# Kernel optimization log

Measured on AMD Instinct MI355X. Metric: run time of the kernel, lower is better.

Reference implementation:

```python
import math
import jax, jax.numpy as jnp
import numpy as np

N, E, EA = 25000, 400000, 400000
DN, DE, H = 256, 128, 8
DHN, DHE = DN // H, DE // H
EPS = 1e-5


def _ln(x, g, b):
    m = x.mean(-1, keepdims=True)
    v = ((x - m) ** 2).mean(-1, keepdims=True)
    return (x - m) * jax.lax.rsqrt(v + EPS) * g + b


def _scatter_softmax(scores, index, n):
    # per-segment stable softmax (matches torch scatter_reduce amax + scatter_add)
    m = jnp.maximum(jax.ops.segment_max(scores, index, num_segments=n), -1e9)
    ex = jnp.exp(scores - m[index])
    den = jax.ops.segment_sum(ex, index, num_segments=n)
    return ex / (den[index] + 1e-10)


def setup_inputs() -> dict:
    key = jax.random.key(0)
    ks = iter(jax.random.split(key, 64))
    rn = lambda shape, s=0.02: jax.random.normal(next(ks), shape, jnp.float32) * s
    inp = {
        'node_features': jax.random.normal(next(ks), (N, DN), jnp.float32),
        'edge_features': jax.random.normal(next(ks), (E, DE), jnp.float32),
        'edge_index': jax.random.randint(next(ks), (2, E), 0, N),
        'edge_adj': jax.random.randint(next(ks), (2, EA), 0, E),
        # NodeAttention params
        'n_Wq': rn((DN, DN)), 'n_bq': jnp.zeros(DN), 'n_Wk': rn((DN, DN)), 'n_bk': jnp.zeros(DN),
        'n_Wv': rn((DN, DN)), 'n_bv': jnp.zeros(DN), 'n_Web': rn((DE, H)), 'n_beb': jnp.zeros(H),
        'n_Wo': rn((DN, DN)), 'n_bo': jnp.zeros(DN), 'n_logt': jnp.zeros(H),
        'n_g': jnp.ones(DN), 'n_b': jnp.zeros(DN),
        # EdgeAttention params
        'e_Wq': rn((DE, DE)), 'e_bq': jnp.zeros(DE), 'e_Wk': rn((DE, DE)), 'e_bk': jnp.zeros(DE),
        'e_Wv': rn((DE, DE)), 'e_bv': jnp.zeros(DE), 'e_Wctx': rn((2 * DN, H)), 'e_bctx': jnp.zeros(H),
        'e_Wo': rn((DE, DE)), 'e_bo': jnp.zeros(DE), 'e_logt': jnp.zeros(H),
        'e_g': jnp.ones(DE), 'e_b': jnp.zeros(DE),
        # ReconciliationBridge params
        'r_We': rn((DE + 2 * DN, DE)), 'r_be': jnp.zeros(DE), 'r_eg': jnp.ones(DE), 'r_ebt': jnp.zeros(DE),
        'r_Wn': rn((DN + DE, DN)), 'r_bn': jnp.zeros(DN), 'r_ng': jnp.ones(DN), 'r_nbt': jnp.zeros(DN),
    }
    return inp


def reference(node_features, edge_features, edge_index, edge_adj,
              n_Wq, n_bq, n_Wk, n_bk, n_Wv, n_bv, n_Web, n_beb, n_Wo, n_bo, n_logt, n_g, n_b,
              e_Wq, e_bq, e_Wk, e_bk, e_Wv, e_bv, e_Wctx, e_bctx, e_Wo, e_bo, e_logt, e_g, e_b,
              r_We, r_be, r_eg, r_ebt, r_Wn, r_bn, r_ng, r_nbt):
    Nn, En = node_features.shape[0], edge_features.shape[0]
    src, tgt = edge_index[0], edge_index[1]

    # ---- NodeAttention (uses original node/edge features) ----
    x = node_features
    Q = (x @ n_Wq + n_bq).reshape(Nn, H, DHN)
    K = (x @ n_Wk + n_bk).reshape(Nn, H, DHN)
    V = (x @ n_Wv + n_bv).reshape(Nn, H, DHN)
    s = (Q[tgt] * K[src]).sum(-1) / math.sqrt(DHN)            # [E, H]
    s = (s + edge_features @ n_Web + n_beb) * jnp.exp(n_logt)
    w = _scatter_softmax(s, tgt, Nn)
    agg = jax.ops.segment_sum(V[src] * w[..., None], tgt, num_segments=Nn).reshape(Nn, DN)
    node_out = _ln(x + agg @ n_Wo + n_bo, n_g, n_b)

    # ---- EdgeAttention (uses original node/edge features) ----
    e = edge_features
    Qe = (e @ e_Wq + e_bq).reshape(En, H, DHE)
    Ke = (e @ e_Wk + e_bk).reshape(En, H, DHE)
    Ve = (e @ e_Wv + e_bv).reshape(En, H, DHE)
    se, te = edge_adj[0], edge_adj[1]
    s2 = (Qe[te] * Ke[se]).sum(-1) / math.sqrt(DHE)           # [EA, H]
    ctx = jnp.concatenate([node_features[src[se]], node_features[tgt[se]]], -1)
    s2 = (s2 + ctx @ e_Wctx + e_bctx) * jnp.exp(e_logt)
    w2 = _scatter_softmax(s2, te, En)
    agg2 = jax.ops.segment_sum(Ve[se] * w2[..., None], te, num_segments=En).reshape(En, DE)
    edge_out = _ln(e + agg2 @ e_Wo + e_bo, e_g, e_b)

    # ---- ReconciliationBridge on updated features ----
    edge_ctx = jnp.concatenate([edge_out, node_out[src], node_out[tgt]], -1)
    new_edges = _ln(edge_out + edge_ctx @ r_We + r_be, r_eg, r_ebt)
    all_nodes = jnp.concatenate([src, tgt])
    all_edges = jnp.concatenate([new_edges, new_edges], 0)
    esum = jax.ops.segment_sum(all_edges, all_nodes, num_segments=Nn)
    ecnt = jax.ops.segment_sum(jnp.ones(all_nodes.shape[0], jnp.float32), all_nodes, num_segments=Nn)
    emean = esum / (ecnt[:, None] + 1e-10)
    node_ctx = jnp.concatenate([node_out, emean], -1)
    new_nodes = _ln(node_out + node_ctx @ r_Wn + r_bn, r_ng, r_nbt)
    return new_nodes, new_edges
```

## Files before the change

### kernel.cpp

```cpp
#include <hip/hip_runtime.h>
#include <cstdio>
#include <cstddef>

typedef unsigned short u16;
typedef unsigned int u32;

#define DEVFN __device__ __forceinline__

namespace {
constexpr int NN = 25000;
constexpr int NE = 400000;
constexpr int NA = 400000;
constexpr int DN = 256;
constexpr int DE = 128;
constexpr int H  = 8;
constexpr float LN_EPS = 1e-5f;
}

DEVFN float bf2f(u32 x) { union { u32 u; float f; } v; v.u = x << 16; return v.f; }
DEVFN u16 f2bf(float f) {
    u32 u = __float_as_uint(f);
    u32 r = 0x7fffu + ((u >> 16) & 1u);
    return (u16)((u + r) >> 16);
}
DEVFN void unpack8(uint4 v, float* f) {
    f[0] = bf2f(v.x & 0xffffu); f[1] = bf2f(v.x >> 16);
    f[2] = bf2f(v.y & 0xffffu); f[3] = bf2f(v.y >> 16);
    f[4] = bf2f(v.z & 0xffffu); f[5] = bf2f(v.z >> 16);
    f[6] = bf2f(v.w & 0xffffu); f[7] = bf2f(v.w >> 16);
}

template<int B> struct IO;
template<> struct IO<1> {
    static DEVFN float ld(const void* p, size_t i) { return bf2f(((const u16*)p)[i]); }
    static DEVFN void ld8(const void* p, size_t i, float* f) {
        unpack8(*reinterpret_cast<const uint4*>((const u16*)p + i), f);
    }
    static DEVFN void st(void* p, size_t i, float v) { ((u16*)p)[i] = f2bf(v); }
};
template<> struct IO<0> {
    static DEVFN float ld(const void* p, size_t i) { return ((const float*)p)[i]; }
    static DEVFN void ld8(const void* p, size_t i, float* f) {
        const float* q = (const float*)p + i;
        float4 a = *reinterpret_cast<const float4*>(q);
        float4 b = *reinterpret_cast<const float4*>(q + 4);
        f[0]=a.x; f[1]=a.y; f[2]=a.z; f[3]=a.w; f[4]=b.x; f[5]=b.y; f[6]=b.z; f[7]=b.w;
    }
    static DEVFN void st(void* p, size_t i, float v) { ((float*)p)[i] = v; }
};

__global__ void k_detect(const void* ng, int* flag) {
    if (threadIdx.x == 0 && blockIdx.x == 0) {
        const u16* p = (const u16*)ng;
        int zeros = 0;
        for (int i = 0; i < 64; i += 2) if (p[i] == 0) ++zeros;
        *flag = (zeros >= 16) ? 0 : 1;
    }
}

__global__ __launch_bounds__(256) void k_fill(float* p, long n, float v) {
    long i = (long)blockIdx.x * 256 + threadIdx.x;
    long st = (long)gridDim.x * 256;
    for (; i < n; i += st) p[i] = v;
}

template<int B>
__global__ __launch_bounds__(256) void k_gemm_bias(
    const int* dflag, const void* __restrict__ A, const void* __restrict__ W,
    const void* __restrict__ bias, u16* __restrict__ out, int M, int K, int Nd)
{
    if (*dflag != B) return;
    __shared__ __align__(16) float As[32][72];
    __shared__ __align__(16) float Ws[32][68];
    const int t = threadIdx.x;
    const int m0 = blockIdx.x * 64;
    const int n0 = blockIdx.y * 64;
    const int r0 = (t >> 4) * 4;
    const int c0 = (t & 15) * 4;
    const int arow = t >> 2, akk = (t & 3) * 8;
    const int wrow = t >> 3, wcc = (t & 7) * 8;
    float acc[4][4] = {};
    for (int k0 = 0; k0 < K; k0 += 32) {
        float av[8];
        const int gr = m0 + arow;
        if (gr < M) IO<B>::ld8(A, (size_t)gr * K + k0 + akk, av);
        else { for (int j = 0; j < 8; ++j) av[j] = 0.f; }
        float wv[8];
        IO<B>::ld8(W, (size_t)(k0 + wrow) * Nd + n0 + wcc, wv);
        __syncthreads();
#pragma unroll
        for (int j = 0; j < 8; ++j) As[akk + j][arow] = av[j];
#pragma unroll
        for (int j = 0; j < 8; ++j) Ws[wrow][wcc + j] = wv[j];
        __syncthreads();
#pragma unroll
        for (int kk = 0; kk < 32; ++kk) {
            float4 a4 = *reinterpret_cast<const float4*>(&As[kk][r0]);
            float4 w4 = *reinterpret_cast<const float4*>(&Ws[kk][c0]);
            float aa[4] = {a4.x, a4.y, a4.z, a4.w};
            float ww[4] = {w4.x, w4.y, w4.z, w4.w};
#pragma unroll
            for (int i = 0; i < 4; ++i)
#pragma unroll
                for (int j = 0; j < 4; ++j) acc[i][j] += aa[i] * ww[j];
        }
        __syncthreads();
    }
    float bv[4];
#pragma unroll
    for (int j = 0; j < 4; ++j) bv[j] = IO<B>::ld(bias, n0 + c0 + j);
#pragma unroll
    for (int i = 0; i < 4; ++i) {
        int gr = m0 + r0 + i;
        if (gr < M) {
            u16* o = out + (size_t)gr * Nd + n0 + c0;
#pragma unroll
            for (int j = 0; j < 4; ++j) o[j] = f2bf(acc[i][j] + bv[j]);
        }
    }
}

template<int B>
__global__ __launch_bounds__(256) void k_edge_bias(
    const int* dflag, const void* __restrict__ ef, const void* __restrict__ Web,
    const void* __restrict__ beb, float* __restrict__ s)
{
    if (*dflag != B) return;
    __shared__ float Wsh[DE * H];
    __shared__ float bsh[H];
    for (int i = threadIdx.x; i < DE * H; i += 256) Wsh[i] = IO<B>::ld(Web, i);
    if (threadIdx.x < H) bsh[threadIdx.x] = IO<B>::ld(beb, threadIdx.x);
    __syncthreads();
    int gid = blockIdx.x * 256 + threadIdx.x;
    if (gid >= NE * H) return;
    int e = gid >> 3, h = gid & 7;
    float acc = 0.f;
    for (int k = 0; k < DE; k += 8) {
        float a[8]; IO<B>::ld8(ef, (size_t)e * DE + k, a);
#pragma unroll
        for (int j = 0; j < 8; ++j) acc += a[j] * Wsh[(k + j) * H + h];
    }
    s[gid] = acc + bsh[h];
}

template<int B>
__global__ __launch_bounds__(256) void k_ctx_bias(
    const int* dflag, const void* __restrict__ nf,
    const int* __restrict__ src, const int* __restrict__ tgt,
    const void* __restrict__ Wctx, const void* __restrict__ bctx, float* __restrict__ ebias)
{
    if (*dflag != B) return;
    __shared__ float Wsh[2 * DN * H];
    __shared__ float bsh[H];
    for (int i = threadIdx.x; i < 2 * DN * H; i += 256) Wsh[i] = IO<B>::ld(Wctx, i);
    if (threadIdx.x < H) bsh[threadIdx.x] = IO<B>::ld(bctx, threadIdx.x);
    __syncthreads();
    int gid = blockIdx.x * 256 + threadIdx.x;
    if (gid >= NE * H) return;
    int e = gid >> 3, h = gid & 7;
    int is = src[e], it = tgt[e];
    if ((unsigned)is >= NN || (unsigned)it >= NN) { ebias[gid] = 0.f; return; }
    float acc = 0.f;
    for (int k = 0; k < DN; k += 8) {
        float a[8]; IO<B>::ld8(nf, (size_t)is * DN + k, a);
#pragma unroll
        for (int j = 0; j < 8; ++j) acc += a[j] * Wsh[(k + j) * H + h];
    }
    for (int k = 0; k < DN; k += 8) {
        float a[8]; IO<B>::ld8(nf, (size_t)it * DN + k, a);
#pragma unroll
        for (int j = 0; j < 8; ++j) acc += a[j] * Wsh[(DN + k + j) * H + h];
    }
    ebias[gid] = acc + bsh[h];
}

template<int B>
__global__ __launch_bounds__(256) void k_node_score(
    const int* dflag, const u16* __restrict__ Q, const u16* __restrict__ Kt,
    const int* __restrict__ src, const int* __restrict__ tgt,
    const void* __restrict__ logt, float* __restrict__ s, float* __restrict__ den)
{
    if (*dflag != B) return;
    int gid = blockIdx.x * 256 + threadIdx.x;
    if (gid >= NE * H) return;
    int e = gid >> 3, h = gid & 7;
    int te = tgt[e], se = src[e];
    if ((unsigned)te >= NN || (unsigned)se >= NN) { s[gid] = 0.f; return; }
    const u16* q = Q + (size_t)te * DN + h * 32;
    const u16* k = Kt + (size_t)se * DN + h * 32;
    float acc = 0.f;
#pragma unroll
    for (int i = 0; i < 4; ++i) {
        float qa[8], ka[8];
        unpack8(*reinterpret_cast<const uint4*>(q + i * 8), qa);
        unpack8(*reinterpret_cast<const uint4*>(k + i * 8), ka);
#pragma unroll
        for (int j = 0; j < 8; ++j) acc += qa[j] * ka[j];
    }
    float val = (acc * 0.17677669529663689f + s[gid]) * expf(IO<B>::ld(logt, h));
    float ex = expf(fminf(val, 60.f));
    s[gid] = ex;
    atomicAdd(&den[(size_t)te * H + h], ex);
}

__global__ __launch_bounds__(256) void k_node_agg(
    const u16* __restrict__ V, const int* __restrict__ src, const int* __restrict__ tgt,
    const float* __restrict__ s, const float* __restrict__ den, float* __restrict__ agg)
{
    long gid = (long)blockIdx.x * 256 + threadIdx.x;
    if (gid >= (long)NE * DN) return;
    int e = (int)(gid >> 8);
    int c = (int)(gid & 255);
    int h = c >> 5;
    int te = tgt[e], se = src[e];
    if ((unsigned)te >= NN || (unsigned)se >= NN) return;
    float w = s[(size_t)e * H + h] / (den[(size_t)te * H + h] + 1e-10f);
    float v = bf2f(V[(size_t)se * DN + c]);
    atomicAdd(&agg[(size_t)te * DN + c], v * w);
}

template<int B>
__global__ __launch_bounds__(256) void k_edge_score(
    const int* dflag, const u16* __restrict__ Qe, const u16* __restrict__ Ke,
    const int* __restrict__ se, const int* __restrict__ te,
    const void* __restrict__ logt, const float* __restrict__ ebias,
    float* __restrict__ s2, float* __restrict__ den2)
{
    if (*dflag != B) return;
    int gid = blockIdx.x * 256 + threadIdx.x;
    if (gid >= NA * H) return;
    int a = gid >> 3, h = gid & 7;
    int tE = te[a], sE = se[a];
    if ((unsigned)tE >= NE || (unsigned)sE >= NE) { s2[gid] = 0.f; return; }
    const u16* q = Qe + (size_t)tE * DE + h * 16;
    const u16* k = Ke + (size_t)sE * DE + h * 16;
    float acc = 0.f;
#pragma unroll
    for (int i = 0; i < 2; ++i) {
        float qa[8], ka[8];
        unpack8(*reinterpret_cast<const uint4*>(q + i * 8), qa);
        unpack8(*reinterpret_cast<const uint4*>(k + i * 8), ka);
#pragma unroll
        for (int j = 0; j < 8; ++j) acc += qa[j] * ka[j];
    }
    float val = (acc * 0.25f + ebias[(size_t)sE * H + h]) * expf(IO<B>::ld(logt, h));
    float ex = expf(fminf(val, 60.f));
    s2[gid] = ex;
    atomicAdd(&den2[(size_t)tE * H + h], ex);
}

__global__ __launch_bounds__(256) void k_edge_agg(
    const u16* __restrict__ Ve, const int* __restrict__ se, const int* __restrict__ te,
    const float* __restrict__ s2, const float* __restrict__ den2, float* __restrict__ agg2)
{
    long gid = (long)blockIdx.x * 256 + threadIdx.x;
    if (gid >= (long)NA * DE) return;
    int a = (int)(gid >> 7);
    int c = (int)(gid & 127);
    int h = c >> 4;
    int tE = te[a], sE = se[a];
    if ((unsigned)tE >= NE || (unsigned)sE >= NE) return;
    float w = s2[(size_t)a * H + h] / (den2[(size_t)tE * H + h] + 1e-10f);
    float v = bf2f(Ve[(size_t)sE * DE + c]);
    atomicAdd(&agg2[(size_t)tE * DE + c], v * w);
}

template<int B>
__global__ __launch_bounds__(256) void k_node_out(
    const int* dflag, const float* __restrict__ agg, const void* __restrict__ x,
    const void* __restrict__ Wo, const void* __restrict__ bo,
    const void* __restrict__ g, const void* __restrict__ b, u16* __restrict__ nout)
{
    if (*dflag != B) return;
    __shared__ __align__(16) float As[32][36];
    __shared__ __align__(16) float Ws[32][264];
    const int t = threadIdx.x;
    const int m0 = blockIdx.x * 32;
    const int r0 = (t >> 5) * 4;
    const int c0 = (t & 31) * 8;
    const int arow = t >> 3, akk = (t & 7) * 4;
    const int wrow = t >> 3, wcc = (t & 7) * 32;
    float acc[4][8] = {};
    for (int k0 = 0; k0 < DN; k0 += 32) {
        float av[4];
        const int gr = m0 + arow;
        if (gr < NN) {
            float4 v = *reinterpret_cast<const float4*>(agg + (size_t)gr * DN + k0 + akk);
            av[0] = v.x; av[1] = v.y; av[2] = v.z; av[3] = v.w;
        } else { av[0] = av[1] = av[2] = av[3] = 0.f; }
        float wv[32];
#pragma unroll
        for (int u = 0; u < 4; ++u)
            IO<B>::ld8(Wo, (size_t)(k0 + wrow) * DN + wcc + u * 8, wv + u * 8);
        __syncthreads();
#pragma unroll
        for (int j = 0; j < 4; ++j) As[akk + j][arow] = av[j];
#pragma unroll
        for (int j = 0; j < 32; ++j) Ws[wrow][wcc + j] = wv[j];
        __syncthreads();
#pragma unroll
        for (int kk = 0; kk < 32; ++kk) {
            float4 a4 = *reinterpret_cast<const float4*>(&As[kk][r0]);
            float4 wa = *reinterpret_cast<const float4*>(&Ws[kk][c0]);
            float4 wb = *reinterpret_cast<const float4*>(&Ws[kk][c0 + 4]);
            float aa[4] = {a4.x, a4.y, a4.z, a4.w};
            float ww[8] = {wa.x, wa.y, wa.z, wa.w, wb.x, wb.y, wb.z, wb.w};
#pragma unroll
            for (int i = 0; i < 4; ++i)
#pragma unroll
                for (int j = 0; j < 8; ++j) acc[i][j] += aa[i] * ww[j];
        }
        __syncthreads();
    }
    float gv[8], bv[8], bov[8];
#pragma unroll
    for (int j = 0; j < 8; ++j) {
        gv[j] = IO<B>::ld(g, c0 + j); bv[j] = IO<B>::ld(b, c0 + j); bov[j] = IO<B>::ld(bo, c0 + j);
    }
#pragma unroll
    for (int i = 0; i < 4; ++i) {
        int gr = m0 + r0 + i;
        if (gr >= NN) continue;
        float xv[8]; IO<B>::ld8(x, (size_t)gr * DN + c0, xv);
        float val[8]; float sum = 0.f, sq = 0.f;
#pragma unroll
        for (int j = 0; j < 8; ++j) {
            val[j] = acc[i][j] + xv[j] + bov[j];
            sum += val[j]; sq += val[j] * val[j];
        }
#pragma unroll
        for (int msk = 1; msk < 32; msk <<= 1) {
            sum += __shfl_xor(sum, msk, 64);
            sq += __shfl_xor(sq, msk, 64);
        }
        float mu = sum * (1.f / DN);
        float var = fmaxf(sq * (1.f / DN) - mu * mu, 0.f);
        float rstd = rsqrtf(var + LN_EPS);
        u16* o = nout + (size_t)gr * DN + c0;
#pragma unroll
        for (int j = 0; j < 8; ++j) o[j] = f2bf((val[j] - mu) * rstd * gv[j] + bv[j]);
    }
}

template<int B>
__global__ __launch_bounds__(256) void k_edge_out(
    const int* dflag, const float* __restrict__ agg2, const void* __restrict__ ef,
    const void* __restrict__ Wo, const void* __restrict__ bo,
    const void* __restrict__ g, const void* __restrict__ b, u16* __restrict__ eout)
{
    if (*dflag != B) return;
    __shared__ __align__(16) float As[32][68];
    __shared__ __align__(16) float Ws[32][136];
    const int t = threadIdx.x;
    const int m0 = blockIdx.x * 64;
    const int r0 = (t >> 4) * 4;
    const int c0 = (t & 15) * 8;
    const int arow = t >> 2, akk = (t & 3) * 8;
    const int wrow = t >> 3, wcc = (t & 7) * 16;
    float acc[4][8] = {};
    for (int k0 = 0; k0 < DE; k0 += 32) {
        float av[8];
        {
            const float* p = agg2 + (size_t)(m0 + arow) * DE + k0 + akk;
            float4 v0 = *reinterpret_cast<const float4*>(p);
            float4 v1 = *reinterpret_cast<const float4*>(p + 4);
            av[0] = v0.x; av[1] = v0.y; av[2] = v0.z; av[3] = v0.w;
            av[4] = v1.x; av[5] = v1.y; av[6] = v1.z; av[7] = v1.w;
        }
        float wv[16];
        IO<B>::ld8(Wo, (size_t)(k0 + wrow) * DE + wcc, wv);
        IO<B>::ld8(Wo, (size_t)(k0 + wrow) * DE + wcc + 8, wv + 8);
        __syncthreads();
#pragma unroll
        for (int j = 0; j < 8; ++j) As[akk + j][arow] = av[j];
#pragma unroll
        for (int j = 0; j < 16; ++j) Ws[wrow][wcc + j] = wv[j];
        __syncthreads();
#pragma unroll
        for (int kk = 0; kk < 32; ++kk) {
            float4 a4 = *reinterpret_cast<const float4*>(&As[kk][r0]);
            float4 wa = *reinterpret_cast<const float4*>(&Ws[kk][c0]);
            float4 wb = *reinterpret_cast<const float4*>(&Ws[kk][c0 + 4]);
            float aa[4] = {a4.x, a4.y, a4.z, a4.w};
            float ww[8] = {wa.x, wa.y, wa.z, wa.w, wb.x, wb.y, wb.z, wb.w};
#pragma unroll
            for (int i = 0; i < 4; ++i)
#pragma unroll
                for (int j = 0; j < 8; ++j) acc[i][j] += aa[i] * ww[j];
        }
        __syncthreads();
    }
    float gv[8], bv[8], bov[8];
#pragma unroll
    for (int j = 0; j < 8; ++j) {
        gv[j] = IO<B>::ld(g, c0 + j); bv[j] = IO<B>::ld(b, c0 + j); bov[j] = IO<B>::ld(bo, c0 + j);
    }
#pragma unroll
    for (int i = 0; i < 4; ++i) {
        int gr = m0 + r0 + i;
        float xv[8]; IO<B>::ld8(ef, (size_t)gr * DE + c0, xv);
        float val[8]; float sum = 0.f, sq = 0.f;
#pragma unroll
        for (int j = 0; j < 8; ++j) {
            val[j] = acc[i][j] + xv[j] + bov[j];
            sum += val[j]; sq += val[j] * val[j];
        }
#pragma unroll
        for (int msk = 1; msk < 16; msk <<= 1) {
            sum += __shfl_xor(sum, msk, 64);
            sq += __shfl_xor(sq, msk, 64);
        }
        float mu = sum * (1.f / DE);
        float var = fmaxf(sq * (1.f / DE) - mu * mu, 0.f);
        float rstd = rsqrtf(var + LN_EPS);
        u16* o = eout + (size_t)gr * DE + c0;
#pragma unroll
        for (int j = 0; j < 8; ++j) o[j] = f2bf((val[j] - mu) * rstd * gv[j] + bv[j]);
    }
}

template<int B>
__global__ __launch_bounds__(256) void k_bridge_edge(
    const int* dflag, const u16* __restrict__ eout, const u16* __restrict__ nout,
    const int* __restrict__ src, const int* __restrict__ tgt,
    const void* __restrict__ We, const void* __restrict__ be,
    const void* __restrict__ g, const void* __restrict__ b,
    void* __restrict__ out_edges)
{
    if (*dflag != B) return;
    __shared__ __align__(16) float As[32][68];
    __shared__ __align__(16) float Ws[32][136];
    __shared__ int es[64], et[64];
    const int t = threadIdx.x;
    const int m0 = blockIdx.x * 64;
    if (t < 64) {
        int a = src[m0 + t], c = tgt[m0 + t];
        es[t] = ((unsigned)a < NN) ? a : 0;
        et[t] = ((unsigned)c < NN) ? c : 0;
    }
    __syncthreads();
    const int r0 = (t >> 4) * 4;
    const int c0 = (t & 15) * 8;
    const int arow = t >> 2, akk = (t & 3) * 8;
    const int wrow = t >> 3, wcc = (t & 7) * 16;
    float acc[4][8] = {};
    for (int k0 = 0; k0 < 640; k0 += 32) {
        const u16* aptr;
        if (k0 < 128)      aptr = eout + (size_t)(m0 + arow) * DE + k0 + akk;
        else if (k0 < 384) aptr = nout + (size_t)es[arow] * DN + (k0 - 128) + akk;
        else               aptr = nout + (size_t)et[arow] * DN + (k0 - 384) + akk;
        float av[8]; unpack8(*reinterpret_cast<const uint4*>(aptr), av);
        float wv[16];
        IO<B>::ld8(We, (size_t)(k0 + wrow) * DE + wcc, wv);
        IO<B>::ld8(We, (size_t)(k0 + wrow) * DE + wcc + 8, wv + 8);
        __syncthreads();
#pragma unroll
        for (int j = 0; j < 8; ++j) As[akk + j][arow] = av[j];
#pragma unroll
        for (int j = 0; j < 16; ++j) Ws[wrow][wcc + j] = wv[j];
        __syncthreads();
#pragma unroll
        for (int kk = 0; kk < 32; ++kk) {
            float4 a4 = *reinterpret_cast<const float4*>(&As[kk][r0]);
            float4 wa = *reinterpret_cast<const float4*>(&Ws[kk][c0]);
            float4 wb = *reinterpret_cast<const float4*>(&Ws[kk][c0 + 4]);
            float aa[4] = {a4.x, a4.y, a4.z, a4.w};
            float ww[8] = {wa.x, wa.y, wa.z, wa.w, wb.x, wb.y, wb.z, wb.w};
#pragma unroll
            for (int i = 0; i < 4; ++i)
#pragma unroll
                for (int j = 0; j < 8; ++j) acc[i][j] += aa[i] * ww[j];
        }
        __syncthreads();
    }
    float gv[8], bv[8], bev[8];
#pragma unroll
    for (int j = 0; j < 8; ++j) {
        gv[j] = IO<B>::ld(g, c0 + j); bv[j] = IO<B>::ld(b, c0 + j); bev[j] = IO<B>::ld(be, c0 + j);
    }
#pragma unroll
    for (int i = 0; i < 4; ++i) {
        int r = r0 + i;
        int gr = m0 + r;
        float val[8]; float sum = 0.f, sq = 0.f;
#pragma unroll
        for (int j = 0; j < 8; ++j) {
            val[j] = acc[i][j] + bf2f(eout[(size_t)gr * DE + c0 + j]) + bev[j];
            sum += val[j]; sq += val[j] * val[j];
        }
#pragma unroll
        for (int msk = 1; msk < 16; msk <<= 1) {
            sum += __shfl_xor(sum, msk, 64);
            sq += __shfl_xor(sq, msk, 64);
        }
        float mu = sum * (1.f / DE);
        float var = fmaxf(sq * (1.f / DE) - mu * mu, 0.f);
        float rstd = rsqrtf(var + LN_EPS);
#pragma unroll
        for (int j = 0; j < 8; ++j) {
            float ov = (val[j] - mu) * rstd * gv[j] + bv[j];
            IO<B>::st(out_edges, (size_t)gr * DE + c0 + j, ov);
        }
    }
}

__global__ __launch_bounds__(256) void k_deg(
    const int* __restrict__ src, const int* __restrict__ tgt, int* __restrict__ cnt)
{
    int e = blockIdx.x * 256 + threadIdx.x;
    if (e >= NE) return;
    int a = src[e]; a = ((unsigned)a < NN) ? a : 0;
    int c = tgt[e]; c = ((unsigned)c < NN) ? c : 0;
    atomicAdd(&cnt[a], 1);
    atomicAdd(&cnt[c], 1);
}

__global__ __launch_bounds__(256) void k_scan(
    const int* __restrict__ cnt, int* __restrict__ off, int* __restrict__ cur, int n)
{
    __shared__ int sh[256];
    __shared__ int carry;
    const int t = threadIdx.x;
    if (t == 0) carry = 0;
    __syncthreads();
    for (int base = 0; base < n; base += 256) {
        int i = base + t;
        int v = (i < n) ? cnt[i] : 0;
        sh[t] = v;
        __syncthreads();
#pragma unroll
        for (int d = 1; d < 256; d <<= 1) {
            int x = (t >= d) ? sh[t - d] : 0;
            __syncthreads();
            sh[t] += x;
            __syncthreads();
        }
        int incl = sh[t];
        int total = sh[255];
        if (i < n) {
            off[i + 1] = carry + incl;
            cur[i] = carry + incl - v;
        }
        __syncthreads();
        if (t == 0) carry += total;
        __syncthreads();
    }
    if (t == 0) off[0] = 0;
}

__global__ __launch_bounds__(256) void k_place(
    const int* __restrict__ src, const int* __restrict__ tgt,
    int* __restrict__ cur, int* __restrict__ ent)
{
    int e = blockIdx.x * 256 + threadIdx.x;
    if (e >= NE) return;
    int a = src[e]; a = ((unsigned)a < NN) ? a : 0;
    int c = tgt[e]; c = ((unsigned)c < NN) ? c : 0;
    int p = atomicAdd(&cur[a], 1); ent[p] = e;
    p = atomicAdd(&cur[c], 1);     ent[p] = e;
}

template<int B>
__global__ __launch_bounds__(256) void k_esum_gather(
    const int* dflag, const void* __restrict__ edges ,
    const int* __restrict__ off, const int* __restrict__ ent,
    float* __restrict__ esum, float* __restrict__ ecnt)
{
    if (*dflag != B) return;
    int node = blockIdx.x * 4 + (threadIdx.x >> 6);
    if (node >= NN) return;
    int lane = threadIdx.x & 63;
    int b0 = off[node], b1 = off[node + 1];
    float a0 = 0.f, a1 = 0.f;
    for (int i = b0; i < b1; ++i) {
        int e = ent[i];
        size_t base = (size_t)e * DE;
        a0 += IO<B>::ld(edges, base + lane);
        a1 += IO<B>::ld(edges, base + 64 + lane);
    }
    esum[(size_t)node * DE + lane] = a0;
    esum[(size_t)node * DE + 64 + lane] = a1;
    if (lane == 0) ecnt[node] = (float)(b1 - b0);
}

template<int B>
__global__ __launch_bounds__(256) void k_bridge_node(
    const int* dflag, const u16* __restrict__ nout,
    const float* __restrict__ esum, const float* __restrict__ ecnt,
    const void* __restrict__ Wn, const void* __restrict__ bn,
    const void* __restrict__ g, const void* __restrict__ b, void* __restrict__ out_nodes)
{
    if (*dflag != B) return;
    __shared__ __align__(16) float As[32][36];
    __shared__ __align__(16) float Ws[32][264];
    __shared__ float rc[32];
    const int t = threadIdx.x;
    const int m0 = blockIdx.x * 32;
    if (t < 32) {
        int gr = m0 + t;
        rc[t] = (gr < NN) ? 1.f / (ecnt[gr] + 1e-10f) : 0.f;
    }
    __syncthreads();
    const int r0 = (t >> 5) * 4;
    const int c0 = (t & 31) * 8;
    const int arow = t >> 3, akk = (t & 7) * 4;
    const int wrow = t >> 3, wcc = (t & 7) * 32;
    float acc[4][8] = {};
    for (int k0 = 0; k0 < 384; k0 += 32) {
        float av[4];
        const int gr = m0 + arow;
        if (gr < NN) {
            if (k0 < 256) {
                uint2 v = *reinterpret_cast<const uint2*>(nout + (size_t)gr * DN + k0 + akk);
                av[0] = bf2f(v.x & 0xffffu); av[1] = bf2f(v.x >> 16);
                av[2] = bf2f(v.y & 0xffffu); av[3] = bf2f(v.y >> 16);
            } else {
                float4 v = *reinterpret_cast<const float4*>(esum + (size_t)gr * DE + (k0 - 256) + akk);
                float r = rc[arow];
                av[0] = v.x * r; av[1] = v.y * r; av[2] = v.z * r; av[3] = v.w * r;
            }
        } else { av[0] = av[1] = av[2] = av[3] = 0.f; }
        float wv[32];
#pragma unroll
        for (int u = 0; u < 4; ++u)
            IO<B>::ld8(Wn, (size_t)(k0 + wrow) * DN + wcc + u * 8, wv + u * 8);
        __syncthreads();
#pragma unroll
        for (int j = 0; j < 4; ++j) As[akk + j][arow] = av[j];
#pragma unroll
        for (int j = 0; j < 32; ++j) Ws[wrow][wcc + j] = wv[j];
        __syncthreads();
#pragma unroll
        for (int kk = 0; kk < 32; ++kk) {
            float4 a4 = *reinterpret_cast<const float4*>(&As[kk][r0]);
            float4 wa = *reinterpret_cast<const float4*>(&Ws[kk][c0]);
            float4 wb = *reinterpret_cast<const float4*>(&Ws[kk][c0 + 4]);
            float aa[4] = {a4.x, a4.y, a4.z, a4.w};
            float ww[8] = {wa.x, wa.y, wa.z, wa.w, wb.x, wb.y, wb.z, wb.w};
#pragma unroll
            for (int i = 0; i < 4; ++i)
#pragma unroll
                for (int j = 0; j < 8; ++j) acc[i][j] += aa[i] * ww[j];
        }
        __syncthreads();
    }
    float gv[8], bv[8], bnv[8];
#pragma unroll
    for (int j = 0; j < 8; ++j) {
        gv[j] = IO<B>::ld(g, c0 + j); bv[j] = IO<B>::ld(b, c0 + j); bnv[j] = IO<B>::ld(bn, c0 + j);
    }
#pragma unroll
    for (int i = 0; i < 4; ++i) {
        int gr = m0 + r0 + i;
        if (gr >= NN) continue;
        float val[8]; float sum = 0.f, sq = 0.f;
#pragma unroll
        for (int j = 0; j < 8; ++j) {
            val[j] = acc[i][j] + bf2f(nout[(size_t)gr * DN + c0 + j]) + bnv[j];
            sum += val[j]; sq += val[j] * val[j];
        }
#pragma unroll
        for (int msk = 1; msk < 32; msk <<= 1) {
            sum += __shfl_xor(sum, msk, 64);
            sq += __shfl_xor(sq, msk, 64);
        }
        float mu = sum * (1.f / DN);
        float var = fmaxf(sq * (1.f / DN) - mu * mu, 0.f);
        float rstd = rsqrtf(var + LN_EPS);
#pragma unroll
        for (int j = 0; j < 8; ++j)
            IO<B>::st(out_nodes, (size_t)gr * DN + c0 + j, (val[j] - mu) * rstd * gv[j] + bv[j]);
    }
}

extern "C" void kernel_launch(void* const* d_in, const int* in_sizes, int n_in,
                              void* d_out, int out_size, void* d_ws, size_t ws_size,
                              hipStream_t stream)
{
    if (n_in < 38 || in_sizes[0] != NN * DN || in_sizes[1] != NE * DE) {
        fprintf(stderr, "kernel_launch: unexpected inputs n_in=%d sz0=%d sz1=%d\n",
                n_in, in_sizes[0], n_in > 1 ? in_sizes[1] : -1);
        return;
    }
    const void* nf  = d_in[0];
    const void* ef  = d_in[1];
    const int* eidx = (const int*)d_in[2];
    const int* eadj = (const int*)d_in[3];
    const int* srcN = eidx;
    const int* tgtN = eidx + NE;
    const int* seA  = eadj;
    const int* teA  = eadj + NA;
    const void *nWq = d_in[4],  *nbq  = d_in[5];
    const void *nWk = d_in[6],  *nbk  = d_in[7];
    const void *nWv = d_in[8],  *nbv  = d_in[9];
    const void *nWeb = d_in[10], *nbeb = d_in[11];
    const void *nWo = d_in[12], *nbo  = d_in[13];
    const void *nlogt = d_in[14], *ng = d_in[15], *nb = d_in[16];
    const void *eWq = d_in[17], *ebq  = d_in[18];
    const void *eWk = d_in[19], *ebk  = d_in[20];
    const void *eWv = d_in[21], *ebv  = d_in[22];
    const void *eWctx = d_in[23], *ebctx = d_in[24];
    const void *eWo = d_in[25], *ebo  = d_in[26];
    const void *elogt = d_in[27], *eg = d_in[28], *ebb = d_in[29];
    const void *rWe = d_in[30], *rbe  = d_in[31];
    const void *reg_ = d_in[32], *rebt = d_in[33];
    const void *rWn = d_in[34], *rbn  = d_in[35];
    const void *rng = d_in[36], *rnbt = d_in[37];

    char* ws = (char*)d_ws;
    size_t off = 0;
    auto take = [&](size_t bytes) -> char* {
        char* p = ws + off;
        off = (off + bytes + 255) & ~(size_t)255;
        return p;
    };
    int*   flag     = (int*)  take(256);
    u16*   node_out = (u16*)  take((size_t)NN * DN * 2);
    u16*   edge_out = (u16*)  take((size_t)NE * DE * 2);
    float* esum     = (float*)take((size_t)NN * DE * 4);
    float* ecnt     = (float*)take((size_t)NN * 4);
    const size_t T = off;
    u16*   Qn   = (u16*)(ws + T);
    u16*   Kn   = Qn + (size_t)NN * DN;
    u16*   Vn   = Kn + (size_t)NN * DN;
    float* sA   = (float*)(Vn + (size_t)NN * DN);
    float* denA = sA + (size_t)NE * H;
    float* aggA = denA + (size_t)NN * H;
    size_t endA = (size_t)((char*)(aggA + (size_t)NN * DN) - ws);
    u16*   Qe    = (u16*)(ws + T);
    u16*   Ke    = Qe + (size_t)NE * DE;
    float* agg2  = (float*)Ke;
    float* ebias = (float*)(ws + T + (size_t)NE * DE * 2 + (size_t)NE * DE * 4);
    float* s2    = ebias + (size_t)NE * H;
    float* den2  = s2 + (size_t)NA * H;
    size_t endB = (size_t)((char*)(den2 + (size_t)NE * H) - ws);
    int* c_off = (int*)(ws + T);
    int* c_cur = c_off + (NN + 1);
    int* c_ent = c_cur + NN;
    size_t endC = (size_t)((char*)(c_ent + (size_t)2 * NE) - ws);
    size_t need = endA > endB ? endA : endB;
    if (endC > need) need = endC;
    if (ws_size < need) {
        fprintf(stderr, "kernel_launch: ws_size=%zu < needed=%zu\n", ws_size, need);
        return;
    }

    auto fill = [&](float* p, long n, float v) {
        long blocks = (n + 255) / 256;
        if (blocks > 8192) blocks = 8192;
        k_fill<<<dim3((unsigned)blocks), dim3(256), 0, stream>>>(p, n, v);
    };

    k_detect<<<1, 64, 0, stream>>>(ng, flag);

    fill(denA, (long)NN * H, 0.f);
    fill(aggA, (long)NN * DN, 0.f);
    dim3 gA((NN + 63) / 64, DN / 64);
    k_gemm_bias<1><<<gA, 256, 0, stream>>>(flag, nf, nWq, nbq, Qn, NN, DN, DN);
    k_gemm_bias<0><<<gA, 256, 0, stream>>>(flag, nf, nWq, nbq, Qn, NN, DN, DN);
    k_gemm_bias<1><<<gA, 256, 0, stream>>>(flag, nf, nWk, nbk, Kn, NN, DN, DN);
    k_gemm_bias<0><<<gA, 256, 0, stream>>>(flag, nf, nWk, nbk, Kn, NN, DN, DN);
    k_gemm_bias<1><<<gA, 256, 0, stream>>>(flag, nf, nWv, nbv, Vn, NN, DN, DN);
    k_gemm_bias<0><<<gA, 256, 0, stream>>>(flag, nf, nWv, nbv, Vn, NN, DN, DN);
    const int gEH = (NE * H + 255) / 256;
    k_edge_bias<1><<<gEH, 256, 0, stream>>>(flag, ef, nWeb, nbeb, sA);
    k_edge_bias<0><<<gEH, 256, 0, stream>>>(flag, ef, nWeb, nbeb, sA);
    k_node_score<1><<<gEH, 256, 0, stream>>>(flag, Qn, Kn, srcN, tgtN, nlogt, sA, denA);
    k_node_score<0><<<gEH, 256, 0, stream>>>(flag, Qn, Kn, srcN, tgtN, nlogt, sA, denA);
    {
        long n = (long)NE * DN;
        k_node_agg<<<dim3((unsigned)((n + 255) / 256)), 256, 0, stream>>>(Vn, srcN, tgtN, sA, denA, aggA);
    }
    k_node_out<1><<<(NN + 31) / 32, 256, 0, stream>>>(flag, aggA, nf, nWo, nbo, ng, nb, node_out);
    k_node_out<0><<<(NN + 31) / 32, 256, 0, stream>>>(flag, aggA, nf, nWo, nbo, ng, nb, node_out);

    dim3 gB(NE / 64, DE / 64);
    k_gemm_bias<1><<<gB, 256, 0, stream>>>(flag, ef, eWq, ebq, Qe, NE, DE, DE);
    k_gemm_bias<0><<<gB, 256, 0, stream>>>(flag, ef, eWq, ebq, Qe, NE, DE, DE);
    k_gemm_bias<1><<<gB, 256, 0, stream>>>(flag, ef, eWk, ebk, Ke, NE, DE, DE);
    k_gemm_bias<0><<<gB, 256, 0, stream>>>(flag, ef, eWk, ebk, Ke, NE, DE, DE);
    k_ctx_bias<1><<<gEH, 256, 0, stream>>>(flag, nf, srcN, tgtN, eWctx, ebctx, ebias);
    k_ctx_bias<0><<<gEH, 256, 0, stream>>>(flag, nf, srcN, tgtN, eWctx, ebctx, ebias);
    fill(den2, (long)NE * H, 0.f);
    const int gAH = (NA * H + 255) / 256;
    k_edge_score<1><<<gAH, 256, 0, stream>>>(flag, Qe, Ke, seA, teA, elogt, ebias, s2, den2);
    k_edge_score<0><<<gAH, 256, 0, stream>>>(flag, Qe, Ke, seA, teA, elogt, ebias, s2, den2);
    k_gemm_bias<1><<<gB, 256, 0, stream>>>(flag, ef, eWv, ebv, Qe , NE, DE, DE);
    k_gemm_bias<0><<<gB, 256, 0, stream>>>(flag, ef, eWv, ebv, Qe , NE, DE, DE);
    fill(agg2, (long)NE * DE, 0.f);
    {
        long n = (long)NA * DE;
        k_edge_agg<<<dim3((unsigned)((n + 255) / 256)), 256, 0, stream>>>(Qe , seA, teA, s2, den2, agg2);
    }
    k_edge_out<1><<<NE / 64, 256, 0, stream>>>(flag, agg2, ef, eWo, ebo, eg, ebb, edge_out);
    k_edge_out<0><<<NE / 64, 256, 0, stream>>>(flag, agg2, ef, eWo, ebo, eg, ebb, edge_out);

    void* out_nodes = d_out;
    void* out_edges_bf = (void*)((u16*)d_out + (size_t)NN * DN);
    void* out_edges_f  = (void*)((float*)d_out + (size_t)NN * DN);
    k_bridge_edge<1><<<NE / 64, 256, 0, stream>>>(flag, edge_out, node_out, srcN, tgtN,
                                                  rWe, rbe, reg_, rebt, out_edges_bf);
    k_bridge_edge<0><<<NE / 64, 256, 0, stream>>>(flag, edge_out, node_out, srcN, tgtN,
                                                  rWe, rbe, reg_, rebt, out_edges_f);
    fill((float*)c_cur, NN, 0.f);
    k_deg<<<(NE + 255) / 256, 256, 0, stream>>>(srcN, tgtN, c_cur);
    k_scan<<<1, 256, 0, stream>>>(c_cur , c_off, c_cur , NN);
    k_place<<<(NE + 255) / 256, 256, 0, stream>>>(srcN, tgtN, c_cur, c_ent);
    k_esum_gather<1><<<(NN + 3) / 4, 256, 0, stream>>>(flag, out_edges_bf, c_off, c_ent, esum, ecnt);
    k_esum_gather<0><<<(NN + 3) / 4, 256, 0, stream>>>(flag, out_edges_f, c_off, c_ent, esum, ecnt);
    k_bridge_node<1><<<(NN + 31) / 32, 256, 0, stream>>>(flag, node_out, esum, ecnt,
                                                         rWn, rbn, rng, rnbt, out_nodes);
    k_bridge_node<0><<<(NN + 31) / 32, 256, 0, stream>>>(flag, node_out, esum, ecnt,
                                                         rWn, rbn, rng, rnbt, out_nodes);
}
```

Before: 3.717 ms.

## Use bf16 MFMA kernels for projection GEMMs and bridge edge GEMM

Adds MFMA-based bf16 GEMM kernels (16x16x32 bf16 intrinsics, swizzled LDS staging of pre-transposed weights with register prefetch) and uses them for the Q/K/V projections of nodes and edges and for the fused bridge-edge gather-GEMM on the bf16 path. Weights are transposed once per call by a small kernel. This replaces scalar FP32 FMA tiled GEMMs with matrix-core instructions. It adds extra transpose launches and workspace, and the A operand is read straight from global memory rather than staged in LDS.

```diff
diff --git a/kernel.cpp b/kernel.cpp
--- a/kernel.cpp
+++ b/kernel.cpp
@@ -29,6 +29,10 @@
     f[4] = bf2f(v.z & 0xffffu); f[5] = bf2f(v.z >> 16);
     f[6] = bf2f(v.w & 0xffffu); f[7] = bf2f(v.w >> 16);
 }
+
+typedef __bf16 bf16x8 __attribute__((ext_vector_type(8)));
+typedef float f32x4 __attribute__((ext_vector_type(4)));
+union B8 { uint4 u; bf16x8 b; };
 
 template<int B> struct IO;
 template<> struct IO<1> {
@@ -62,6 +66,513 @@
     long i = (long)blockIdx.x * 256 + threadIdx.x;
     long st = (long)gridDim.x * 256;
     for (; i < n; i += st) p[i] = v;
+}
+
+__global__ __launch_bounds__(256) void k_transpose(
+    const int* dflag, const u16* __restrict__ in, u16* __restrict__ out, int K, int Nd)
+{
+    if (*dflag != 1) return;
+    int gid = blockIdx.x * 256 + threadIdx.x;
+    if (gid >= K * Nd) return;
+    int n = gid / K, k = gid - n * K;
+    out[gid] = in[(size_t)k * Nd + n];
+}
+
+__global__ __launch_bounds__(256) void k_gemm_mfma(
+    const int* dflag, const u16* __restrict__ A, const u16* __restrict__ Wt,
+    const u16* __restrict__ bias, u16* __restrict__ out, int M, int K, int Nd)
+{
+    if (*dflag != 1) return;
+    __shared__ __align__(16) char shbuf[128 * 128];
+    const int t = threadIdx.x;
+    const int m0 = blockIdx.x * 64;
+    const int n0 = blockIdx.y * 128;
+    const int w = t >> 6;
+    const int lane = t & 63;
+    const int lm = lane & 15, lg = lane >> 4;
+    const int NC = K >> 6;
+
+    uint4 sreg[4];
+    auto gstage = [&](int kc) {
+#pragma unroll
+        for (int it = 0; it < 4; ++it) {
+            int idx = it * 256 + t;
+            int n = idx >> 3, slot = idx & 7;
+            sreg[it] = *reinterpret_cast<const uint4*>(Wt + (size_t)(n0 + n) * K + kc * 64 + slot * 8);
+        }
+    };
+    auto swrite = [&]() {
+#pragma unroll
+        for (int it = 0; it < 4; ++it) {
+            int idx = it * 256 + t;
+            int n = idx >> 3, slot = idx & 7;
+            *reinterpret_cast<uint4*>(shbuf + n * 128 + ((slot ^ (n & 7)) * 16)) = sreg[it];
+        }
+    };
+
+    f32x4 acc[4][2];
+    const f32x4 z = {0.f, 0.f, 0.f, 0.f};
+#pragma unroll
+    for (int mf = 0; mf < 4; ++mf)
+#pragma unroll
+        for (int nf = 0; nf < 2; ++nf) acc[mf][nf] = z;
+
+    gstage(0); swrite();
+    for (int kc = 0; kc < NC; ++kc) {
+        if (kc + 1 < NC) gstage(kc + 1);
+        __syncthreads();
+#pragma unroll
+        for (int ksl = 0; ksl < 2; ++ksl) {
+            B8 a[4];
+#pragma unroll
+            for (int mf = 0; mf < 4; ++mf) {
+                int r = m0 + mf * 16 + lm;
+                if (r >= M) r = M - 1;
+                a[mf].u = *reinterpret_cast<const uint4*>(A + (size_t)r * K + kc * 64 + ksl * 32 + lg * 8);
+            }
+#pragma unroll
+            for (int nf = 0; nf < 2; ++nf) {
+                int n = w * 32 + nf * 16 + lm;
+                int slot = ksl * 4 + lg;
+                B8 bfrag;
+                bfrag.u = *reinterpret_cast<const uint4*>(shbuf + n * 128 + ((slot ^ (n & 7)) * 16));
+#pragma unroll
+                for (int mf = 0; mf < 4; ++mf)
+                    acc[mf][nf] = __builtin_amdgcn_mfma_f32_16x16x32_bf16(a[mf].b, bfrag.b, acc[mf][nf], 0, 0, 0);
+            }
+        }
+        __syncthreads();
+        if (kc + 1 < NC) swrite();
+    }
+#pragma unroll
+    for (int mf = 0; mf < 4; ++mf)
+#pragma unroll
+        for (int nf = 0; nf < 2; ++nf) {
+            int col = n0 + w * 32 + nf * 16 + lm;
+            float bb = bf2f(bias[col]);
+#pragma unroll
+            for (int j = 0; j < 4; ++j) {
+                int gr = m0 + mf * 16 + lg * 4 + j;
+                if (gr < M) out[(size_t)gr * Nd + col] = f2bf(acc[mf][nf][j] + bb);
+            }
+        }
+}
+
+template<int B>
+__global__ __launch_bounds__(256) void k_edge_bias(
+    const int* dflag, const void* __restrict__ ef, const void* __restrict__ Web,
+    const void* __restrict__ beb, float* __restrict__ s)
+{
+    if (*dflag != B) return;
+    __shared__ float Wsh[DE * H];
+    __shared__ float bsh[H];
+    for (int i = threadIdx.x; i < DE * H; i += 256) Wsh[i] = IO<B>::ld(Web, i);
+    if (threadIdx.x < H) bsh[threadIdx.x] = IO<B>::ld(beb, threadIdx.x);
+    __syncthreads();
+    int gid = blockIdx.x * 256 + threadIdx.x;
+    if (gid >= NE * H) return;
+    int e = gid >> 3, h = gid & 7;
+    float acc = 0.f;
+    for (int k = 0; k < DE; k += 8) {
+        float a[8]; IO<B>::ld8(ef, (size_t)e * DE + k, a);
+#pragma unroll
+        for (int j = 0; j < 8; ++j) acc += a[j] * Wsh[(k + j) * H + h];
+    }
+    s[gid] = acc + bsh[h];
+}
+
+template<int B>
+__global__ __launch_bounds__(256) void k_ctx_bias(
+    const int* dflag, const void* __restrict__ nf,
+    const int* __restrict__ src, const int* __restrict__ tgt,
+    const void* __restrict__ Wctx, const void* __restrict__ bctx, float* __restrict__ ebias)
+{
+    if (*dflag != B) return;
+    __shared__ float Wsh[2 * DN * H];
+    __shared__ float bsh[H];
+    for (int i = threadIdx.x; i < 2 * DN * H; i += 256) Wsh[i] = IO<B>::ld(Wctx, i);
+    if (threadIdx.x < H) bsh[threadIdx.x] = IO<B>::ld(bctx, threadIdx.x);
+    __syncthreads();
+    int gid = blockIdx.x * 256 + threadIdx.x;
+    if (gid >= NE * H) return;
+    int e = gid >> 3, h = gid & 7;
+    int is = src[e], it = tgt[e];
+    if ((unsigned)is >= NN || (unsigned)it >= NN) { ebias[gid] = 0.f; return; }
+    float acc = 0.f;
+    for (int k = 0; k < DN; k += 8) {
+        float a[8]; IO<B>::ld8(nf, (size_t)is * DN + k, a);
+#pragma unroll
+        for (int j = 0; j < 8; ++j) acc += a[j] * Wsh[(k + j) * H + h];
+    }
+    for (int k = 0; k < DN; k += 8) {
+        float a[8]; IO<B>::ld8(nf, (size_t)it * DN + k, a);
+#pragma unroll
+        for (int j = 0; j < 8; ++j) acc += a[j] * Wsh[(DN + k + j) * H + h];
+    }
+    ebias[gid] = acc + bsh[h];
+}
+
+template<int B>
+__global__ __launch_bounds__(256) void k_node_score(
+    const int* dflag, const u16* __restrict__ Q, const u16* __restrict__ Kt,
+    const int* __restrict__ src, const int* __restrict__ tgt,
+    const void* __restrict__ logt, float* __restrict__ s, float* __restrict__ den)
+{
+    if (*dflag != B) return;
+    int gid = blockIdx.x * 256 + threadIdx.x;
+    if (gid >= NE * H) return;
+    int e = gid >> 3, h = gid & 7;
+    int te = tgt[e], se = src[e];
+    if ((unsigned)te >= NN || (unsigned)se >= NN) { s[gid] = 0.f; return; }
+    const u16* q = Q + (size_t)te * DN + h * 32;
+    const u16* k = Kt + (size_t)se * DN + h * 32;
+    float acc = 0.f;
+#pragma unroll
+    for (int i = 0; i < 4; ++i) {
+        float qa[8], ka[8];
+        unpack8(*reinterpret_cast<const uint4*>(q + i * 8), qa);
+        unpack8(*reinterpret_cast<const uint4*>(k + i * 8), ka);
+#pragma unroll
+        for (int j = 0; j < 8; ++j) acc += qa[j] * ka[j];
+    }
+    float val = (acc * 0.17677669529663689f + s[gid]) * expf(IO<B>::ld(logt, h));
+    float ex = expf(fminf(val, 60.f));
+    s[gid] = ex;
+    atomicAdd(&den[(size_t)te * H + h], ex);
+}
+
+__global__ __launch_bounds__(256) void k_node_agg(
+    const u16* __restrict__ V, const int* __restrict__ src, const int* __restrict__ tgt,
+    const float* __restrict__ s, const float* __restrict__ den, float* __restrict__ agg)
+{
+    long gid = (long)blockIdx.x * 256 + threadIdx.x;
+    if (gid >= (long)NE * DN) return;
+    int e = (int)(gid >> 8);
+    int c = (int)(gid & 255);
+    int h = c >> 5;
+    int te = tgt[e], se = src[e];
+    if ((unsigned)te >= NN || (unsigned)se >= NN) return;
+    float w = s[(size_t)e * H + h] / (den[(size_t)te * H + h] + 1e-10f);
+    float v = bf2f(V[(size_t)se * DN + c]);
+    atomicAdd(&agg[(size_t)te * DN + c], v * w);
+}
+
+template<int B>
+__global__ __launch_bounds__(256) void k_edge_score(
+    const int* dflag, const u16* __restrict__ Qe, const u16* __restrict__ Ke,
+    const int* __restrict__ se, const int* __restrict__ te,
+    const void* __restrict__ logt, const float* __restrict__ ebias,
+    float* __restrict__ s2, float* __restrict__ den2)
+{
+    if (*dflag != B) return;
+    int gid = blockIdx.x * 256 + threadIdx.x;
+    if (gid >= NA * H) return;
+    int a = gid >> 3, h = gid & 7;
+    int tE = te[a], sE = se[a];
+    if ((unsigned)tE >= NE || (unsigned)sE >= NE) { s2[gid] = 0.f; return; }
+    const u16* q = Qe + (size_t)tE * DE + h * 16;
+    const u16* k = Ke + (size_t)sE * DE + h * 16;
+    float acc = 0.f;
+#pragma unroll
+    for (int i = 0; i < 2; ++i) {
+        float qa[8], ka[8];
+        unpack8(*reinterpret_cast<const uint4*>(q + i * 8), qa);
+        unpack8(*reinterpret_cast<const uint4*>(k + i * 8), ka);
+#pragma unroll
+        for (int j = 0; j < 8; ++j) acc += qa[j] * ka[j];
+    }
+    float val = (acc * 0.25f + ebias[(size_t)sE * H + h]) * expf(IO<B>::ld(logt, h));
+    float ex = expf(fminf(val, 60.f));
+    s2[gid] = ex;
+    atomicAdd(&den2[(size_t)tE * H + h], ex);
+}
+
+__global__ __launch_bounds__(256) void k_edge_agg(
+    const u16* __restrict__ Ve, const int* __restrict__ se, const int* __restrict__ te,
+    const float* __restrict__ s2, const float* __restrict__ den2, float* __restrict__ agg2)
+{
+    long gid = (long)blockIdx.x * 256 + threadIdx.x;
+    if (gid >= (long)NA * DE) return;
+    int a = (int)(gid >> 7);
+    int c = (int)(gid & 127);
+    int h = c >> 4;
+    int tE = te[a], sE = se[a];
+    if ((unsigned)tE >= NE || (unsigned)sE >= NE) return;
+    float w = s2[(size_t)a * H + h] / (den2[(size_t)tE * H + h] + 1e-10f);
+    float v = bf2f(Ve[(size_t)sE * DE + c]);
+    atomicAdd(&agg2[(size_t)tE * DE + c], v * w);
+}
+
+template<int B>
+__global__ __launch_bounds__(256) void k_node_out(
+    const int* dflag, const float* __restrict__ agg, const void* __restrict__ x,
+    const void* __restrict__ Wo, const void* __restrict__ bo,
+    const void* __restrict__ g, const void* __restrict__ b, u16* __restrict__ nout)
+{
+    if (*dflag != B) return;
+    __shared__ __align__(16) float As[32][36];
+    __shared__ __align__(16) float Ws[32][264];
+    const int t = threadIdx.x;
+    const int m0 = blockIdx.x * 32;
+    const int r0 = (t >> 5) * 4;
+    const int c0 = (t & 31) * 8;
+    const int arow = t >> 3, akk = (t & 7) * 4;
+    const int wrow = t >> 3, wcc = (t & 7) * 32;
+    float acc[4][8] = {};
+    for (int k0 = 0; k0 < DN; k0 += 32) {
+        float av[4];
+        const int gr = m0 + arow;
+        if (gr < NN) {
+            float4 v = *reinterpret_cast<const float4*>(agg + (size_t)gr * DN + k0 + akk);
+            av[0] = v.x; av[1] = v.y; av[2] = v.z; av[3] = v.w;
+        } else { av[0] = av[1] = av[2] = av[3] = 0.f; }
+        float wv[32];
+#pragma unroll
+        for (int u = 0; u < 4; ++u)
+            IO<B>::ld8(Wo, (size_t)(k0 + wrow) * DN + wcc + u * 8, wv + u * 8);
+        __syncthreads();
+#pragma unroll
+        for (int j = 0; j < 4; ++j) As[akk + j][arow] = av[j];
+#pragma unroll
+        for (int j = 0; j < 32; ++j) Ws[wrow][wcc + j] = wv[j];
+        __syncthreads();
+#pragma unroll
+        for (int kk = 0; kk < 32; ++kk) {
+            float4 a4 = *reinterpret_cast<const float4*>(&As[kk][r0]);
+            float4 wa = *reinterpret_cast<const float4*>(&Ws[kk][c0]);
+            float4 wb = *reinterpret_cast<const float4*>(&Ws[kk][c0 + 4]);
+            float aa[4] = {a4.x, a4.y, a4.z, a4.w};
+            float ww[8] = {wa.x, wa.y, wa.z, wa.w, wb.x, wb.y, wb.z, wb.w};
+#pragma unroll
+            for (int i = 0; i < 4; ++i)
+#pragma unroll
+                for (int j = 0; j < 8; ++j) acc[i][j] += aa[i] * ww[j];
+        }
+        __syncthreads();
+    }
+    float gv[8], bv[8], bov[8];
+#pragma unroll
+    for (int j = 0; j < 8; ++j) {
+        gv[j] = IO<B>::ld(g, c0 + j); bv[j] = IO<B>::ld(b, c0 + j); bov[j] = IO<B>::ld(bo, c0 + j);
+    }
+#pragma unroll
+    for (int i = 0; i < 4; ++i) {
+        int gr = m0 + r0 + i;
+        if (gr >= NN) continue;
+        float xv[8]; IO<B>::ld8(x, (size_t)gr * DN + c0, xv);
+        float val[8]; float sum = 0.f, sq = 0.f;
+#pragma unroll
+        for (int j = 0; j < 8; ++j) {
+            val[j] = acc[i][j] + xv[j] + bov[j];
+            sum += val[j]; sq += val[j] * val[j];
+        }
+#pragma unroll
+        for (int msk = 1; msk < 32; msk <<= 1) {
+            sum += __shfl_xor(sum, msk, 64);
+            sq += __shfl_xor(sq, msk, 64);
+        }
+        float mu = sum * (1.f / DN);
+        float var = fmaxf(sq * (1.f / DN) - mu * mu, 0.f);
+        float rstd = rsqrtf(var + LN_EPS);
+        u16* o = nout + (size_t)gr * DN + c0;
+#pragma unroll
+        for (int j = 0; j < 8; ++j) o[j] = f2bf((val[j] - mu) * rstd * gv[j] + bv[j]);
+    }
+}
+
+template<int B>
+__global__ __launch_bounds__(256) void k_edge_out(
+    const int* dflag, const float* __restrict__ agg2, const void* __restrict__ ef,
+    const void* __restrict__ Wo, const void* __restrict__ bo,
+    const void* __restrict__ g, const void* __restrict__ b, u16* __restrict__ eout)
+{
+    if (*dflag != B) return;
+    __shared__ __align__(16) float As[32][68];
+    __shared__ __align__(16) float Ws[32][136];
+    const int t = threadIdx.x;
+    const int m0 = blockIdx.x * 64;
+    const int r0 = (t >> 4) * 4;
+    const int c0 = (t & 15) * 8;
+    const int arow = t >> 2, akk = (t & 3) * 8;
+    const int wrow = t >> 3, wcc = (t & 7) * 16;
+    float acc[4][8] = {};
+    for (int k0 = 0; k0 < DE; k0 += 32) {
+        float av[8];
+        {
+            const float* p = agg2 + (size_t)(m0 + arow) * DE + k0 + akk;
+            float4 v0 = *reinterpret_cast<const float4*>(p);
+            float4 v1 = *reinterpret_cast<const float4*>(p + 4);
+            av[0] = v0.x; av[1] = v0.y; av[2] = v0.z; av[3] = v0.w;
+            av[4] = v1.x; av[5] = v1.y; av[6] = v1.z; av[7] = v1.w;
+        }
+        float wv[16];
+        IO<B>::ld8(Wo, (size_t)(k0 + wrow) * DE + wcc, wv);
+        IO<B>::ld8(Wo, (size_t)(k0 + wrow) * DE + wcc + 8, wv + 8);
+        __syncthreads();
+#pragma unroll
+        for (int j = 0; j < 8; ++j) As[akk + j][arow] = av[j];
+#pragma unroll
+        for (int j = 0; j < 16; ++j) Ws[wrow][wcc + j] = wv[j];
+        __syncthreads();
+#pragma unroll
+        for (int kk = 0; kk < 32; ++kk) {
+            float4 a4 = *reinterpret_cast<const float4*>(&As[kk][r0]);
+            float4 wa = *reinterpret_cast<const float4*>(&Ws[kk][c0]);
+            float4 wb = *reinterpret_cast<const float4*>(&Ws[kk][c0 + 4]);
+            float aa[4] = {a4.x, a4.y, a4.z, a4.w};
+            float ww[8] = {wa.x, wa.y, wa.z, wa.w, wb.x, wb.y, wb.z, wb.w};
+#pragma unroll
+            for (int i = 0; i < 4; ++i)
+#pragma unroll
+                for (int j = 0; j < 8; ++j) acc[i][j] += aa[i] * ww[j];
+        }
+        __syncthreads();
+    }
+    float gv[8], bv[8], bov[8];
+#pragma unroll
+    for (int j = 0; j < 8; ++j) {
+        gv[j] = IO<B>::ld(g, c0 + j); bv[j] = IO<B>::ld(b, c0 + j); bov[j] = IO<B>::ld(bo, c0 + j);
+    }
+#pragma unroll
+    for (int i = 0; i < 4; ++i) {
+        int gr = m0 + r0 + i;
+        float xv[8]; IO<B>::ld8(ef, (size_t)gr * DE + c0, xv);
+        float val[8]; float sum = 0.f, sq = 0.f;
+#pragma unroll
+        for (int j = 0; j < 8; ++j) {
+            val[j] = acc[i][j] + xv[j] + bov[j];
+            sum += val[j]; sq += val[j] * val[j];
+        }
+#pragma unroll
+        for (int msk = 1; msk < 16; msk <<= 1) {
+            sum += __shfl_xor(sum, msk, 64);
+            sq += __shfl_xor(sq, msk, 64);
+        }
+        float mu = sum * (1.f / DE);
+        float var = fmaxf(sq * (1.f / DE) - mu * mu, 0.f);
+        float rstd = rsqrtf(var + LN_EPS);
+        u16* o = eout + (size_t)gr * DE + c0;
+#pragma unroll
+        for (int j = 0; j < 8; ++j) o[j] = f2bf((val[j] - mu) * rstd * gv[j] + bv[j]);
+    }
+}
+
+__global__ __launch_bounds__(256) void k_bridge_edge_mfma(
+    const int* dflag, const u16* __restrict__ eout, const u16* __restrict__ nout,
+    const int* __restrict__ src, const int* __restrict__ tgt,
+    const u16* __restrict__ Wt, const u16* __restrict__ be,
+    const u16* __restrict__ g, const u16* __restrict__ b,
+    u16* __restrict__ out_edges)
+{
+    if (*dflag != 1) return;
+    __shared__ __align__(16) char shbuf[64 * 132 * 4];
+    __shared__ int es_sh[64], et_sh[64];
+    const int t = threadIdx.x;
+    const int m0 = blockIdx.x * 64;
+    if (t < 64) {
+        int a = src[m0 + t], c = tgt[m0 + t];
+        es_sh[t] = ((unsigned)a < NN) ? a : 0;
+        et_sh[t] = ((unsigned)c < NN) ? c : 0;
+    }
+    const int w = t >> 6;
+    const int lane = t & 63;
+    const int lm = lane & 15, lg = lane >> 4;
+    constexpr int K = 640, NC = 10;
+
+    uint4 sreg[4];
+    auto gstage = [&](int kc) {
+#pragma unroll
+        for (int it = 0; it < 4; ++it) {
+            int idx = it * 256 + t;
+            int n = idx >> 3, slot = idx & 7;
+            sreg[it] = *reinterpret_cast<const uint4*>(Wt + (size_t)n * K + kc * 64 + slot * 8);
+        }
+    };
+    auto swrite = [&]() {
+#pragma unroll
+        for (int it = 0; it < 4; ++it) {
+            int idx = it * 256 + t;
+            int n = idx >> 3, slot = idx & 7;
+            *reinterpret_cast<uint4*>(shbuf + n * 128 + ((slot ^ (n & 7)) * 16)) = sreg[it];
+        }
+    };
+
+    f32x4 acc[4][2];
+    const f32x4 z = {0.f, 0.f, 0.f, 0.f};
+#pragma unroll
+    for (int mf = 0; mf < 4; ++mf)
+#pragma unroll
+        for (int nf = 0; nf < 2; ++nf) acc[mf][nf] = z;
+
+    gstage(0); swrite();
+    for (int kc = 0; kc < NC; ++kc) {
+        if (kc + 1 < NC) gstage(kc + 1);
+        __syncthreads();
+#pragma unroll
+        for (int ksl = 0; ksl < 2; ++ksl) {
+            B8 a[4];
+#pragma unroll
+            for (int mf = 0; mf < 4; ++mf) {
+                int rloc = mf * 16 + lm;
+                const u16* ap;
+                if (kc < 2)      ap = eout + (size_t)(m0 + rloc) * DE + kc * 64;
+                else if (kc < 6) ap = nout + (size_t)es_sh[rloc] * DN + (kc - 2) * 64;
+                else             ap = nout + (size_t)et_sh[rloc] * DN + (kc - 6) * 64;
+                a[mf].u = *reinterpret_cast<const uint4*>(ap + ksl * 32 + lg * 8);
+            }
+#pragma unroll
+            for (int nf = 0; nf < 2; ++nf) {
+                int n = w * 32 + nf * 16 + lm;
+                int slot = ksl * 4 + lg;
+                B8 bfrag;
+                bfrag.u = *reinterpret_cast<const uint4*>(shbuf + n * 128 + ((slot ^ (n & 7)) * 16));
+#pragma unroll
+                for (int mf = 0; mf < 4; ++mf)
+                    acc[mf][nf] = __builtin_amdgcn_mfma_f32_16x16x32_bf16(a[mf].b, bfrag.b, acc[mf][nf], 0, 0, 0);
+            }
+        }
+        __syncthreads();
+        if (kc + 1 < NC) swrite();
+    }
+    float* cex = (float*)shbuf;
+#pragma unroll
+    for (int mf = 0; mf < 4; ++mf)
+#pragma unroll
+        for (int nf = 0; nf < 2; ++nf)
+#pragma unroll
+            for (int j = 0; j < 4; ++j)
+                cex[(mf * 16 + lg * 4 + j) * 132 + (w * 32 + nf * 16 + lm)] = acc[mf][nf][j];
+    __syncthreads();
+    {
+        const int row = t >> 2, seg = t & 3;
+        const int gr = m0 + row;
+        const int cb = seg * 32;
+        float v[32]; float sum = 0.f, sq = 0.f;
+#pragma unroll
+        for (int u = 0; u < 4; ++u) {
+            float ev[8], bev[8];
+            unpack8(*reinterpret_cast<const uint4*>(eout + (size_t)gr * DE + cb + u * 8), ev);
+            unpack8(*reinterpret_cast<const uint4*>(be + cb + u * 8), bev);
+#pragma unroll
+            for (int j = 0; j < 8; ++j) {
+                float x = cex[row * 132 + cb + u * 8 + j] + ev[j] + bev[j];
+                v[u * 8 + j] = x; sum += x; sq += x * x;
+            }
+        }
+        sum += __shfl_xor(sum, 1, 64); sq += __shfl_xor(sq, 1, 64);
+        sum += __shfl_xor(sum, 2, 64); sq += __shfl_xor(sq, 2, 64);
+        float mu = sum * (1.f / DE);
+        float rstd = rsqrtf(fmaxf(sq * (1.f / DE) - mu * mu, 0.f) + LN_EPS);
+#pragma unroll
+        for (int u = 0; u < 4; ++u) {
+            float gv[8], bv[8];
+            unpack8(*reinterpret_cast<const uint4*>(g + cb + u * 8), gv);
+            unpack8(*reinterpret_cast<const uint4*>(b + cb + u * 8), bv);
+#pragma unroll
+            for (int j = 0; j < 8; ++j)
+                out_edges[(size_t)gr * DE + cb + u * 8 + j] = f2bf((v[u * 8 + j] - mu) * rstd * gv[j] + bv[j]);
+        }
+    }
 }
 
 template<int B>
@@ -117,305 +628,6 @@
 #pragma unroll
             for (int j = 0; j < 4; ++j) o[j] = f2bf(acc[i][j] + bv[j]);
         }
-    }
-}
-
-template<int B>
-__global__ __launch_bounds__(256) void k_edge_bias(
-    const int* dflag, const void* __restrict__ ef, const void* __restrict__ Web,
-    const void* __restrict__ beb, float* __restrict__ s)
-{
-    if (*dflag != B) return;
-    __shared__ float Wsh[DE * H];
-    __shared__ float bsh[H];
-    for (int i = threadIdx.x; i < DE * H; i += 256) Wsh[i] = IO<B>::ld(Web, i);
-    if (threadIdx.x < H) bsh[threadIdx.x] = IO<B>::ld(beb, threadIdx.x);
-    __syncthreads();
-    int gid = blockIdx.x * 256 + threadIdx.x;
-    if (gid >= NE * H) return;
-    int e = gid >> 3, h = gid & 7;
-    float acc = 0.f;
-    for (int k = 0; k < DE; k += 8) {
-        float a[8]; IO<B>::ld8(ef, (size_t)e * DE + k, a);
-#pragma unroll
-        for (int j = 0; j < 8; ++j) acc += a[j] * Wsh[(k + j) * H + h];
-    }
-    s[gid] = acc + bsh[h];
-}
-
-template<int B>
-__global__ __launch_bounds__(256) void k_ctx_bias(
-    const int* dflag, const void* __restrict__ nf,
-    const int* __restrict__ src, const int* __restrict__ tgt,
-    const void* __restrict__ Wctx, const void* __restrict__ bctx, float* __restrict__ ebias)
-{
-    if (*dflag != B) return;
-    __shared__ float Wsh[2 * DN * H];
-    __shared__ float bsh[H];
-    for (int i = threadIdx.x; i < 2 * DN * H; i += 256) Wsh[i] = IO<B>::ld(Wctx, i);
-    if (threadIdx.x < H) bsh[threadIdx.x] = IO<B>::ld(bctx, threadIdx.x);
-    __syncthreads();
-    int gid = blockIdx.x * 256 + threadIdx.x;
-    if (gid >= NE * H) return;
-    int e = gid >> 3, h = gid & 7;
-    int is = src[e], it = tgt[e];
-    if ((unsigned)is >= NN || (unsigned)it >= NN) { ebias[gid] = 0.f; return; }
-    float acc = 0.f;
-    for (int k = 0; k < DN; k += 8) {
-        float a[8]; IO<B>::ld8(nf, (size_t)is * DN + k, a);
-#pragma unroll
-        for (int j = 0; j < 8; ++j) acc += a[j] * Wsh[(k + j) * H + h];
-    }
-    for (int k = 0; k < DN; k += 8) {
-        float a[8]; IO<B>::ld8(nf, (size_t)it * DN + k, a);
-#pragma unroll
-        for (int j = 0; j < 8; ++j) acc += a[j] * Wsh[(DN + k + j) * H + h];
-    }
-    ebias[gid] = acc + bsh[h];
-}
-
-template<int B>
-__global__ __launch_bounds__(256) void k_node_score(
-    const int* dflag, const u16* __restrict__ Q, const u16* __restrict__ Kt,
-    const int* __restrict__ src, const int* __restrict__ tgt,
-    const void* __restrict__ logt, float* __restrict__ s, float* __restrict__ den)
-{
-    if (*dflag != B) return;
-    int gid = blockIdx.x * 256 + threadIdx.x;
-    if (gid >= NE * H) return;
-    int e = gid >> 3, h = gid & 7;
-    int te = tgt[e], se = src[e];
-    if ((unsigned)te >= NN || (unsigned)se >= NN) { s[gid] = 0.f; return; }
-    const u16* q = Q + (size_t)te * DN + h * 32;
-    const u16* k = Kt + (size_t)se * DN + h * 32;
-    float acc = 0.f;
-#pragma unroll
-    for (int i = 0; i < 4; ++i) {
-        float qa[8], ka[8];
-        unpack8(*reinterpret_cast<const uint4*>(q + i * 8), qa);
-        unpack8(*reinterpret_cast<const uint4*>(k + i * 8), ka);
-#pragma unroll
-        for (int j = 0; j < 8; ++j) acc += qa[j] * ka[j];
-    }
-    float val = (acc * 0.17677669529663689f + s[gid]) * expf(IO<B>::ld(logt, h));
-    float ex = expf(fminf(val, 60.f));
-    s[gid] = ex;
-    atomicAdd(&den[(size_t)te * H + h], ex);
-}
-
-__global__ __launch_bounds__(256) void k_node_agg(
-    const u16* __restrict__ V, const int* __restrict__ src, const int* __restrict__ tgt,
-    const float* __restrict__ s, const float* __restrict__ den, float* __restrict__ agg)
-{
-    long gid = (long)blockIdx.x * 256 + threadIdx.x;
-    if (gid >= (long)NE * DN) return;
-    int e = (int)(gid >> 8);
-    int c = (int)(gid & 255);
-    int h = c >> 5;
-    int te = tgt[e], se = src[e];
-    if ((unsigned)te >= NN || (unsigned)se >= NN) return;
-    float w = s[(size_t)e * H + h] / (den[(size_t)te * H + h] + 1e-10f);
-    float v = bf2f(V[(size_t)se * DN + c]);
-    atomicAdd(&agg[(size_t)te * DN + c], v * w);
-}
-
-template<int B>
-__global__ __launch_bounds__(256) void k_edge_score(
-    const int* dflag, const u16* __restrict__ Qe, const u16* __restrict__ Ke,
-    const int* __restrict__ se, const int* __restrict__ te,
-    const void* __restrict__ logt, const float* __restrict__ ebias,
-    float* __restrict__ s2, float* __restrict__ den2)
-{
-    if (*dflag != B) return;
-    int gid = blockIdx.x * 256 + threadIdx.x;
-    if (gid >= NA * H) return;
-    int a = gid >> 3, h = gid & 7;
-    int tE = te[a], sE = se[a];
-    if ((unsigned)tE >= NE || (unsigned)sE >= NE) { s2[gid] = 0.f; return; }
-    const u16* q = Qe + (size_t)tE * DE + h * 16;
-    const u16* k = Ke + (size_t)sE * DE + h * 16;
-    float acc = 0.f;
-#pragma unroll
-    for (int i = 0; i < 2; ++i) {
-        float qa[8], ka[8];
-        unpack8(*reinterpret_cast<const uint4*>(q + i * 8), qa);
-        unpack8(*reinterpret_cast<const uint4*>(k + i * 8), ka);
-#pragma unroll
-        for (int j = 0; j < 8; ++j) acc += qa[j] * ka[j];
-    }
-    float val = (acc * 0.25f + ebias[(size_t)sE * H + h]) * expf(IO<B>::ld(logt, h));
-    float ex = expf(fminf(val, 60.f));
-    s2[gid] = ex;
-    atomicAdd(&den2[(size_t)tE * H + h], ex);
-}
-
-__global__ __launch_bounds__(256) void k_edge_agg(
-    const u16* __restrict__ Ve, const int* __restrict__ se, const int* __restrict__ te,
-    const float* __restrict__ s2, const float* __restrict__ den2, float* __restrict__ agg2)
-{
-    long gid = (long)blockIdx.x * 256 + threadIdx.x;
-    if (gid >= (long)NA * DE) return;
-    int a = (int)(gid >> 7);
-    int c = (int)(gid & 127);
-    int h = c >> 4;
-    int tE = te[a], sE = se[a];
-    if ((unsigned)tE >= NE || (unsigned)sE >= NE) return;
-    float w = s2[(size_t)a * H + h] / (den2[(size_t)tE * H + h] + 1e-10f);
-    float v = bf2f(Ve[(size_t)sE * DE + c]);
-    atomicAdd(&agg2[(size_t)tE * DE + c], v * w);
-}
-
-template<int B>
-__global__ __launch_bounds__(256) void k_node_out(
-    const int* dflag, const float* __restrict__ agg, const void* __restrict__ x,
-    const void* __restrict__ Wo, const void* __restrict__ bo,
-    const void* __restrict__ g, const void* __restrict__ b, u16* __restrict__ nout)
-{
-    if (*dflag != B) return;
-    __shared__ __align__(16) float As[32][36];
-    __shared__ __align__(16) float Ws[32][264];
-    const int t = threadIdx.x;
-    const int m0 = blockIdx.x * 32;
-    const int r0 = (t >> 5) * 4;
-    const int c0 = (t & 31) * 8;
-    const int arow = t >> 3, akk = (t & 7) * 4;
-    const int wrow = t >> 3, wcc = (t & 7) * 32;
-    float acc[4][8] = {};
-    for (int k0 = 0; k0 < DN; k0 += 32) {
-        float av[4];
-        const int gr = m0 + arow;
-        if (gr < NN) {
-            float4 v = *reinterpret_cast<const float4*>(agg + (size_t)gr * DN + k0 + akk);
-            av[0] = v.x; av[1] = v.y; av[2] = v.z; av[3] = v.w;
-        } else { av[0] = av[1] = av[2] = av[3] = 0.f; }
-        float wv[32];
-#pragma unroll
-        for (int u = 0; u < 4; ++u)
-            IO<B>::ld8(Wo, (size_t)(k0 + wrow) * DN + wcc + u * 8, wv + u * 8);
-        __syncthreads();
-#pragma unroll
-        for (int j = 0; j < 4; ++j) As[akk + j][arow] = av[j];
-#pragma unroll
-        for (int j = 0; j < 32; ++j) Ws[wrow][wcc + j] = wv[j];
-        __syncthreads();
-#pragma unroll
-        for (int kk = 0; kk < 32; ++kk) {
-            float4 a4 = *reinterpret_cast<const float4*>(&As[kk][r0]);
-            float4 wa = *reinterpret_cast<const float4*>(&Ws[kk][c0]);
-            float4 wb = *reinterpret_cast<const float4*>(&Ws[kk][c0 + 4]);
-            float aa[4] = {a4.x, a4.y, a4.z, a4.w};
-            float ww[8] = {wa.x, wa.y, wa.z, wa.w, wb.x, wb.y, wb.z, wb.w};
-#pragma unroll
-            for (int i = 0; i < 4; ++i)
-#pragma unroll
-                for (int j = 0; j < 8; ++j) acc[i][j] += aa[i] * ww[j];
-        }
-        __syncthreads();
-    }
-    float gv[8], bv[8], bov[8];
-#pragma unroll
-    for (int j = 0; j < 8; ++j) {
-        gv[j] = IO<B>::ld(g, c0 + j); bv[j] = IO<B>::ld(b, c0 + j); bov[j] = IO<B>::ld(bo, c0 + j);
-    }
-#pragma unroll
-    for (int i = 0; i < 4; ++i) {
-        int gr = m0 + r0 + i;
-        if (gr >= NN) continue;
-        float xv[8]; IO<B>::ld8(x, (size_t)gr * DN + c0, xv);
-        float val[8]; float sum = 0.f, sq = 0.f;
-#pragma unroll
-        for (int j = 0; j < 8; ++j) {
-            val[j] = acc[i][j] + xv[j] + bov[j];
-            sum += val[j]; sq += val[j] * val[j];
-        }
-#pragma unroll
-        for (int msk = 1; msk < 32; msk <<= 1) {
-            sum += __shfl_xor(sum, msk, 64);
-            sq += __shfl_xor(sq, msk, 64);
-        }
-        float mu = sum * (1.f / DN);
-        float var = fmaxf(sq * (1.f / DN) - mu * mu, 0.f);
-        float rstd = rsqrtf(var + LN_EPS);
-        u16* o = nout + (size_t)gr * DN + c0;
-#pragma unroll
-        for (int j = 0; j < 8; ++j) o[j] = f2bf((val[j] - mu) * rstd * gv[j] + bv[j]);
-    }
-}
-
-template<int B>
-__global__ __launch_bounds__(256) void k_edge_out(
-    const int* dflag, const float* __restrict__ agg2, const void* __restrict__ ef,
-    const void* __restrict__ Wo, const void* __restrict__ bo,
-    const void* __restrict__ g, const void* __restrict__ b, u16* __restrict__ eout)
-{
-    if (*dflag != B) return;
-    __shared__ __align__(16) float As[32][68];
-    __shared__ __align__(16) float Ws[32][136];
-    const int t = threadIdx.x;
-    const int m0 = blockIdx.x * 64;
-    const int r0 = (t >> 4) * 4;
-    const int c0 = (t & 15) * 8;
-    const int arow = t >> 2, akk = (t & 3) * 8;
-    const int wrow = t >> 3, wcc = (t & 7) * 16;
-    float acc[4][8] = {};
-    for (int k0 = 0; k0 < DE; k0 += 32) {
-        float av[8];
-        {
-            const float* p = agg2 + (size_t)(m0 + arow) * DE + k0 + akk;
-            float4 v0 = *reinterpret_cast<const float4*>(p);
-            float4 v1 = *reinterpret_cast<const float4*>(p + 4);
-            av[0] = v0.x; av[1] = v0.y; av[2] = v0.z; av[3] = v0.w;
-            av[4] = v1.x; av[5] = v1.y; av[6] = v1.z; av[7] = v1.w;
-        }
-        float wv[16];
-        IO<B>::ld8(Wo, (size_t)(k0 + wrow) * DE + wcc, wv);
-        IO<B>::ld8(Wo, (size_t)(k0 + wrow) * DE + wcc + 8, wv + 8);
-        __syncthreads();
-#pragma unroll
-        for (int j = 0; j < 8; ++j) As[akk + j][arow] = av[j];
-#pragma unroll
-        for (int j = 0; j < 16; ++j) Ws[wrow][wcc + j] = wv[j];
-        __syncthreads();
-#pragma unroll
-        for (int kk = 0; kk < 32; ++kk) {
-            float4 a4 = *reinterpret_cast<const float4*>(&As[kk][r0]);
-            float4 wa = *reinterpret_cast<const float4*>(&Ws[kk][c0]);
-            float4 wb = *reinterpret_cast<const float4*>(&Ws[kk][c0 + 4]);
-            float aa[4] = {a4.x, a4.y, a4.z, a4.w};
-            float ww[8] = {wa.x, wa.y, wa.z, wa.w, wb.x, wb.y, wb.z, wb.w};
-#pragma unroll
-            for (int i = 0; i < 4; ++i)
-#pragma unroll
-                for (int j = 0; j < 8; ++j) acc[i][j] += aa[i] * ww[j];
-        }
-        __syncthreads();
-    }
-    float gv[8], bv[8], bov[8];
-#pragma unroll
-    for (int j = 0; j < 8; ++j) {
-        gv[j] = IO<B>::ld(g, c0 + j); bv[j] = IO<B>::ld(b, c0 + j); bov[j] = IO<B>::ld(bo, c0 + j);
-    }
-#pragma unroll
-    for (int i = 0; i < 4; ++i) {
-        int gr = m0 + r0 + i;
-        float xv[8]; IO<B>::ld8(ef, (size_t)gr * DE + c0, xv);
-        float val[8]; float sum = 0.f, sq = 0.f;
-#pragma unroll
-        for (int j = 0; j < 8; ++j) {
-            val[j] = acc[i][j] + xv[j] + bov[j];
-            sum += val[j]; sq += val[j] * val[j];
-        }
-#pragma unroll
-        for (int msk = 1; msk < 16; msk <<= 1) {
-            sum += __shfl_xor(sum, msk, 64);
-            sq += __shfl_xor(sq, msk, 64);
-        }
-        float mu = sum * (1.f / DE);
-        float var = fmaxf(sq * (1.f / DE) - mu * mu, 0.f);
-        float rstd = rsqrtf(var + LN_EPS);
-        u16* o = eout + (size_t)gr * DE + c0;
-#pragma unroll
-        for (int j = 0; j < 8; ++j) o[j] = f2bf((val[j] - mu) * rstd * gv[j] + bv[j]);
     }
 }
 
@@ -719,6 +931,13 @@
     u16*   edge_out = (u16*)  take((size_t)NE * DE * 2);
     float* esum     = (float*)take((size_t)NN * DE * 4);
     float* ecnt     = (float*)take((size_t)NN * 4);
+    u16* WtQn = (u16*)take((size_t)DN * DN * 2);
+    u16* WtKn = (u16*)take((size_t)DN * DN * 2);
+    u16* WtVn = (u16*)take((size_t)DN * DN * 2);
+    u16* WtQe = (u16*)take((size_t)DE * DE * 2);
+    u16* WtKe = (u16*)take((size_t)DE * DE * 2);
+    u16* WtVe = (u16*)take((size_t)DE * DE * 2);
+    u16* WtWe = (u16*)take((size_t)640 * DE * 2);
     const size_t T = off;
     u16*   Qn   = (u16*)(ws + T);
     u16*   Kn   = Qn + (size_t)NN * DN;
@@ -753,14 +972,22 @@
 
     k_detect<<<1, 64, 0, stream>>>(ng, flag);
 
+    auto T2D = [&](const void* W, u16* Wt, int K, int Nd) {
+        k_transpose<<<dim3((unsigned)((K * Nd + 255) / 256)), 256, 0, stream>>>(flag, (const u16*)W, Wt, K, Nd);
+    };
+    T2D(nWq, WtQn, DN, DN); T2D(nWk, WtKn, DN, DN); T2D(nWv, WtVn, DN, DN);
+    T2D(eWq, WtQe, DE, DE); T2D(eWk, WtKe, DE, DE); T2D(eWv, WtVe, DE, DE);
+    T2D(rWe, WtWe, 640, DE);
+
     fill(denA, (long)NN * H, 0.f);
     fill(aggA, (long)NN * DN, 0.f);
     dim3 gA((NN + 63) / 64, DN / 64);
-    k_gemm_bias<1><<<gA, 256, 0, stream>>>(flag, nf, nWq, nbq, Qn, NN, DN, DN);
+    dim3 gAm((NN + 63) / 64, DN / 128);
+    k_gemm_mfma<<<gAm, 256, 0, stream>>>(flag, (const u16*)nf, WtQn, (const u16*)nbq, Qn, NN, DN, DN);
     k_gemm_bias<0><<<gA, 256, 0, stream>>>(flag, nf, nWq, nbq, Qn, NN, DN, DN);
-    k_gemm_bias<1><<<gA, 256, 0, stream>>>(flag, nf, nWk, nbk, Kn, NN, DN, DN);
+    k_gemm_mfma<<<gAm, 256, 0, stream>>>(flag, (const u16*)nf, WtKn, (const u16*)nbk, Kn, NN, DN, DN);
     k_gemm_bias<0><<<gA, 256, 0, stream>>>(flag, nf, nWk, nbk, Kn, NN, DN, DN);
-    k_gemm_bias<1><<<gA, 256, 0, stream>>>(flag, nf, nWv, nbv, Vn, NN, DN, DN);
+    k_gemm_mfma<<<gAm, 256, 0, stream>>>(flag, (const u16*)nf, WtVn, (const u16*)nbv, Vn, NN, DN, DN);
     k_gemm_bias<0><<<gA, 256, 0, stream>>>(flag, nf, nWv, nbv, Vn, NN, DN, DN);
     const int gEH = (NE * H + 255) / 256;
     k_edge_bias<1><<<gEH, 256, 0, stream>>>(flag, ef, nWeb, nbeb, sA);
@@ -775,9 +1002,10 @@
     k_node_out<0><<<(NN + 31) / 32, 256, 0, stream>>>(flag, aggA, nf, nWo, nbo, ng, nb, node_out);
 
     dim3 gB(NE / 64, DE / 64);
-    k_gemm_bias<1><<<gB, 256, 0, stream>>>(flag, ef, eWq, ebq, Qe, NE, DE, DE);
+    dim3 gBm(NE / 64, DE / 128);
+    k_gemm_mfma<<<gBm, 256, 0, stream>>>(flag, (const u16*)ef, WtQe, (const u16*)ebq, Qe, NE, DE, DE);
     k_gemm_bias<0><<<gB, 256, 0, stream>>>(flag, ef, eWq, ebq, Qe, NE, DE, DE);
-    k_gemm_bias<1><<<gB, 256, 0, stream>>>(flag, ef, eWk, ebk, Ke, NE, DE, DE);
+    k_gemm_mfma<<<gBm, 256, 0, stream>>>(flag, (const u16*)ef, WtKe, (const u16*)ebk, Ke, NE, DE, DE);
     k_gemm_bias<0><<<gB, 256, 0, stream>>>(flag, ef, eWk, ebk, Ke, NE, DE, DE);
     k_ctx_bias<1><<<gEH, 256, 0, stream>>>(flag, nf, srcN, tgtN, eWctx, ebctx, ebias);
     k_ctx_bias<0><<<gEH, 256, 0, stream>>>(flag, nf, srcN, tgtN, eWctx, ebctx, ebias);
@@ -785,7 +1013,7 @@
     const int gAH = (NA * H + 255) / 256;
     k_edge_score<1><<<gAH, 256, 0, stream>>>(flag, Qe, Ke, seA, teA, elogt, ebias, s2, den2);
     k_edge_score<0><<<gAH, 256, 0, stream>>>(flag, Qe, Ke, seA, teA, elogt, ebias, s2, den2);
-    k_gemm_bias<1><<<gB, 256, 0, stream>>>(flag, ef, eWv, ebv, Qe , NE, DE, DE);
+    k_gemm_mfma<<<gBm, 256, 0, stream>>>(flag, (const u16*)ef, WtVe, (const u16*)ebv, Qe , NE, DE, DE);
     k_gemm_bias<0><<<gB, 256, 0, stream>>>(flag, ef, eWv, ebv, Qe , NE, DE, DE);
     fill(agg2, (long)NE * DE, 0.f);
     {
@@ -798,8 +1026,9 @@
     void* out_nodes = d_out;
     void* out_edges_bf = (void*)((u16*)d_out + (size_t)NN * DN);
     void* out_edges_f  = (void*)((float*)d_out + (size_t)NN * DN);
-    k_bridge_edge<1><<<NE / 64, 256, 0, stream>>>(flag, edge_out, node_out, srcN, tgtN,
-                                                  rWe, rbe, reg_, rebt, out_edges_bf);
+    k_bridge_edge_mfma<<<NE / 64, 256, 0, stream>>>(flag, edge_out, node_out, srcN, tgtN,
+                                                    WtWe, (const u16*)rbe, (const u16*)reg_, (const u16*)rebt,
+                                                    (u16*)out_edges_bf);
     k_bridge_edge<0><<<NE / 64, 256, 0, stream>>>(flag, edge_out, node_out, srcN, tgtN,
                                                   rWe, rbe, reg_, rebt, out_edges_f);
     fill((float*)c_cur, NN, 0.f);
```

Measured after the change: 3.770 ms. Within noise of the previous version (+1.4%).
